# Performance work log

Hardware: AMD Instinct MI355X
Metric: run time of the kernel (lower is better)

## Reference

```python
import jax, jax.numpy as jnp
import numpy as np

N = 50000        # nodes
E = 800000       # edges (edge-nodes of the line graph)
LGE = 1600000    # line-graph edges
F_NODE = 256     # node feature dim
T = 64           # timestamp/edge feature dim
HID = 128        # hidden size
OUT = 64         # out size
SLOPE = 0.2      # leaky relu negative slope used in EdgeGCN / attention


def _glorot(key, shape):
    lim = jnp.sqrt(6.0 / (shape[0] + shape[1]))
    return jax.random.uniform(key, shape, jnp.float32, -lim, lim)


def setup_inputs() -> dict:
    key = jax.random.key(0)
    ks = jax.random.split(key, 24)
    inp = {
        "x": jax.random.normal(ks[0], (N, F_NODE), jnp.float32),
        "et": jax.random.normal(ks[1], (E, T), jnp.float32),
        "H": jax.random.randint(ks[2], (2, E), 0, N),
        "raw_edge_index": jax.random.randint(ks[3], (2, E), 0, N),
        "lg_edge_index": jax.random.randint(ks[4], (2, LGE), 0, E),
        # TSAEncoder: two SAGE-style layers on the line graph (T->HID->HID)
        "W_tsa1_s": _glorot(ks[5], (T, HID)),
        "W_tsa1_n": _glorot(ks[6], (T, HID)),
        "W_tsa2_s": _glorot(ks[7], (HID, HID)),
        "W_tsa2_n": _glorot(ks[8], (HID, HID)),
        # EdgeToNodeConv + EdgeGCN output linear
        "W_etn": _glorot(ks[9], (HID, HID)),
        "W_eg_lin": _glorot(ks[10], (HID, HID)),
        # edge_aggr SAGE (num_layers-1 = 1 layer)
        "W_ea_s": _glorot(ks[11], (HID, HID)),
        "W_ea_n": _glorot(ks[12], (HID, HID)),
        # attr_node_model SAGE (2 layers)
        "W_an1_s": _glorot(ks[13], (F_NODE, HID)),
        "W_an1_n": _glorot(ks[14], (F_NODE, HID)),
        "W_an2_s": _glorot(ks[15], (HID, HID)),
        "W_an2_n": _glorot(ks[16], (HID, HID)),
        # MixAttention
        "Wq": _glorot(ks[17], (HID, HID)),
        "Wk": _glorot(ks[18], (HID, HID)),
        "Wv": _glorot(ks[19], (HID, HID)),
        # final classifier
        "W_out": _glorot(ks[20], (HID, OUT)),
    }
    return inp


def _sage(h, src, dst, Ws, Wn, n):
    # mean-aggregator SAGE conv: self transform + mean of in-neighbors
    deg = jnp.clip(jax.ops.segment_sum(jnp.ones(src.shape[0], h.dtype), dst, num_segments=n), 1.0)
    nbr = jax.ops.segment_sum(h[src], dst, num_segments=n) / deg[:, None]
    return h @ Ws + nbr @ Wn


def reference(x, et, H, raw_edge_index, lg_edge_index,
              W_tsa1_s, W_tsa1_n, W_tsa2_s, W_tsa2_n,
              W_etn, W_eg_lin, W_ea_s, W_ea_n,
              W_an1_s, W_an1_n, W_an2_s, W_an2_n,
              Wq, Wk, Wv, W_out):
    src_lg, dst_lg = lg_edge_index[0], lg_edge_index[1]
    src, dst = raw_edge_index[0], raw_edge_index[1]

    # ---- EdgeGCN: TSAEncoder over line graph (edges as nodes) ----
    h = jax.nn.relu(_sage(et, src_lg, dst_lg, W_tsa1_s, W_tsa1_n, E))
    h = _sage(h, src_lg, dst_lg, W_tsa2_s, W_tsa2_n, E)          # [E, HID]

    # ---- EdgeToNodeConv: scatter edge reprs to both incident nodes (mean) ----
    ones_e = jnp.ones(E, h.dtype)
    agg = (jax.ops.segment_sum(h, H[0], num_segments=N)
           + jax.ops.segment_sum(h, H[1], num_segments=N))        # [N, HID]
    deg = jnp.clip(jax.ops.segment_sum(ones_e, H[0], num_segments=N)
                   + jax.ops.segment_sum(ones_e, H[1], num_segments=N), 1.0)
    node_e = (agg / deg[:, None]) @ W_etn
    edge_repr = jax.nn.leaky_relu(node_e, negative_slope=SLOPE) @ W_eg_lin  # [N, HID]

    # ---- edge_aggr: 1-layer SAGE over raw graph ----
    aggr_edge = _sage(edge_repr, src, dst, W_ea_s, W_ea_n, N)     # [N, HID]

    # ---- attr_node_model: 2-layer SAGE ----
    hn = jax.nn.relu(_sage(x, src, dst, W_an1_s, W_an1_n, N))
    hn = _sage(hn, src, dst, W_an2_s, W_an2_n, N)                 # [N, HID]

    # ---- MixAttention: edge-indexed cross attention (node queries, edge-repr keys/values) ----
    q = hn @ Wq
    k = aggr_edge @ Wk
    v = aggr_edge @ Wv
    score = jax.nn.leaky_relu(
        jnp.sum(q[dst] * k[src], axis=-1) / jnp.sqrt(jnp.asarray(HID, q.dtype)),
        negative_slope=SLOPE)                                     # [E]
    m = jax.ops.segment_max(score, dst, num_segments=N)
    m = jnp.where(jnp.isfinite(m), m, 0.0)
    ex = jnp.exp(score - m[dst])
    den = jnp.clip(jax.ops.segment_sum(ex, dst, num_segments=N), 1e-9)
    alpha = ex / den[dst]
    out = hn + jax.ops.segment_sum(alpha[:, None] * v[src], dst, num_segments=N)

    return jax.nn.log_softmax(out @ W_out, axis=1)                # [N, OUT]
```

## Files before the change

kernel.cpp:

```cpp
#include <hip/hip_runtime.h>
#include <cstddef>

static constexpr int Nn   = 50000;
static constexpr int Ee   = 800000;
static constexpr int LGEe = 1600000;

typedef __attribute__((ext_vector_type(8))) short bf16x8;
typedef __attribute__((ext_vector_type(4))) float f32x4;

__device__ __forceinline__ float bf2f(unsigned int u16) {
  return __uint_as_float(u16 << 16);
}
__device__ __forceinline__ unsigned int f2bf(float f) {
  unsigned int u = __float_as_uint(f);
  u += 0x7fffu + ((u >> 16) & 1u);
  return u >> 16;
}

__global__ __launch_bounds__(256)
void k_count_direct(const int* __restrict__ idx, int* __restrict__ cnt, int n) {
  int i = blockIdx.x * 256 + threadIdx.x;
  if (i < n) atomicAdd(&cnt[idx[i]], 1);
}
__global__ __launch_bounds__(256)
void k_count_comp(const int* __restrict__ Hrow, const int* __restrict__ dlg,
                  int* __restrict__ cnt, int n) {
  int i = blockIdx.x * 256 + threadIdx.x;
  if (i < n) atomicAdd(&cnt[Hrow[dlg[i]]], 1);
}
__global__ __launch_bounds__(256)
void k_scan1(const int* __restrict__ in, int* __restrict__ out,
             int* __restrict__ bsum, int n) {
  __shared__ int sd[256];
  int tid = threadIdx.x;
  int base = blockIdx.x * 1024 + tid * 4;
  int4 v = {0, 0, 0, 0};
  if (base < n) v = *(const int4*)(in + base);
  int s = v.x + v.y + v.z + v.w;
  sd[tid] = s; __syncthreads();
  for (int off = 1; off < 256; off <<= 1) {
    int t_ = (tid >= off) ? sd[tid - off] : 0; __syncthreads();
    sd[tid] += t_; __syncthreads();
  }
  int excl = sd[tid] - s;
  if (base < n) {
    int4 o; o.x = excl; o.y = o.x + v.x; o.z = o.y + v.y; o.w = o.z + v.z;
    *(int4*)(out + base) = o;
  }
  if (tid == 255) bsum[blockIdx.x] = sd[255];
}
__global__ __launch_bounds__(1024)
void k_scan2(int* __restrict__ b, int nb) {
  __shared__ int sd[1024];
  int tid = threadIdx.x;
  int v = (tid < nb) ? b[tid] : 0;
  sd[tid] = v; __syncthreads();
  for (int off = 1; off < 1024; off <<= 1) {
    int t_ = (tid >= off) ? sd[tid - off] : 0; __syncthreads();
    sd[tid] += t_; __syncthreads();
  }
  if (tid < nb) b[tid] = sd[tid] - v;
}
__global__ __launch_bounds__(256)
void k_scan3(int* __restrict__ out, const int* __restrict__ bsum, int n, int total) {
  int i = blockIdx.x * 256 + threadIdx.x;
  if (i < n) out[i] += bsum[i >> 10];
  if (i == 0) out[n] = total;
}
__global__ __launch_bounds__(256)
void k_fillA(const int* __restrict__ dlg, const int* __restrict__ slg,
             const int* __restrict__ ptr, int* __restrict__ cur,
             int* __restrict__ ent, int n) {
  int m = blockIdx.x * 256 + threadIdx.x;
  if (m >= n) return;
  int d = dlg[m];
  int pos = ptr[d] + atomicAdd(&cur[d], 1);
  ent[pos] = slg[m];
}
__global__ __launch_bounds__(256)
void k_fillB(const int* __restrict__ Hrow, const int* __restrict__ dlg,
             const int* __restrict__ slg, const int* __restrict__ ptrA,
             const int* __restrict__ ptrB, int* __restrict__ cur,
             int* __restrict__ entS, float* __restrict__ entW, int n) {
  int m = blockIdx.x * 256 + threadIdx.x;
  if (m >= n) return;
  int d = dlg[m];
  int seg = Hrow[d];
  int pos = ptrB[seg] + atomicAdd(&cur[seg], 1);
  entS[pos] = slg[m];
  int la = ptrA[d + 1] - ptrA[d];
  entW[pos] = 1.0f / (float)max(la, 1);
}
__global__ __launch_bounds__(256)
void k_fillC(const int* __restrict__ Hrow, const int* __restrict__ ptr,
             int* __restrict__ cur, int* __restrict__ ent, int n) {
  int e = blockIdx.x * 256 + threadIdx.x;
  if (e >= n) return;
  int seg = Hrow[e];
  int pos = ptr[seg] + atomicAdd(&cur[seg], 1);
  ent[pos] = e;
}
__global__ __launch_bounds__(256)
void k_fillD(const int* __restrict__ dstA, const int* __restrict__ srcA,
             const int* __restrict__ ptr, int* __restrict__ cur,
             int* __restrict__ ent, int n) {
  int e = blockIdx.x * 256 + threadIdx.x;
  if (e >= n) return;
  int seg = dstA[e];
  int pos = ptr[seg] + atomicAdd(&cur[seg], 1);
  ent[pos] = srcA[e];
}
__global__ __launch_bounds__(256)
void k_rdeg(const int* __restrict__ ptr, float* __restrict__ r, int n) {
  int i = blockIdx.x * 256 + threadIdx.x;
  if (i < n) r[i] = 1.0f / fmaxf((float)(ptr[i + 1] - ptr[i]), 1.0f);
}

__global__ __launch_bounds__(256)
void k_gemm128(int M, const float* __restrict__ A, int K,
               const float* __restrict__ W, const float* __restrict__ dgA,
               int reluA, int act, float* __restrict__ C)
{
  __shared__ float sA[32][132];
  __shared__ float sW[32][132];
  const int t = threadIdx.x, tr = t >> 4, tc = t & 15;
  const int row0 = blockIdx.x * 128;
  float acc[8][8];
  #pragma unroll
  for (int i = 0; i < 8; ++i)
    #pragma unroll
    for (int j = 0; j < 8; ++j) acc[i][j] = 0.f;

  #pragma unroll 1
  for (int k0 = 0; k0 < K; k0 += 32) {
    __syncthreads();
    #pragma unroll
    for (int j = 0; j < 4; ++j) {
      int idx = t * 4 + j * 1024;
      int r = idx >> 5, kk = idx & 31;
      int gr = row0 + r; if (gr > M - 1) gr = M - 1;
      float4 va = *(const float4*)(A + (size_t)gr * K + k0 + kk);
      if (reluA) {
        va.x = fmaxf(va.x, 0.f); va.y = fmaxf(va.y, 0.f);
        va.z = fmaxf(va.z, 0.f); va.w = fmaxf(va.w, 0.f);
      }
      if (dgA) {
        float sc = dgA[gr];
        va.x *= sc; va.y *= sc; va.z *= sc; va.w *= sc;
      }
      sA[kk + 0][r] = va.x; sA[kk + 1][r] = va.y;
      sA[kk + 2][r] = va.z; sA[kk + 3][r] = va.w;
    }
    #pragma unroll
    for (int j = 0; j < 4; ++j) {
      int idx = t * 4 + j * 1024;
      int kk = idx >> 7, c = idx & 127;
      *(float4*)&sW[kk][c] = *(const float4*)(W + (size_t)(k0 + kk) * 128 + c);
    }
    __syncthreads();
    #pragma unroll
    for (int kk = 0; kk < 32; ++kk) {
      float a[8], w[8];
      *(float4*)&a[0] = *(const float4*)&sA[kk][tr * 4];
      *(float4*)&a[4] = *(const float4*)&sA[kk][64 + tr * 4];
      *(float4*)&w[0] = *(const float4*)&sW[kk][tc * 4];
      *(float4*)&w[4] = *(const float4*)&sW[kk][64 + tc * 4];
      #pragma unroll
      for (int i = 0; i < 8; ++i)
        #pragma unroll
        for (int j = 0; j < 8; ++j)
          acc[i][j] = fmaf(a[i], w[j], acc[i][j]);
    }
  }
  #pragma unroll 1
  for (int i = 0; i < 8; ++i) {
    int gr = row0 + (i & 4) * 16 + tr * 4 + (i & 3);
    if (gr >= M) continue;
    float o[8];
    #pragma unroll
    for (int j = 0; j < 8; ++j) {
      float vv = acc[i][j];
      if (act == 1)      vv = fmaxf(vv, 0.f);
      else if (act == 2) vv = vv > 0.f ? vv : vv * 0.2f;
      o[j] = vv;
    }
    float* p = C + (size_t)gr * 128;
    *(float4*)(p + tc * 4)      = *(const float4*)&o[0];
    *(float4*)(p + 64 + tc * 4) = *(const float4*)&o[4];
  }
}

__global__ __launch_bounds__(256)
void k_tsa1(const float* __restrict__ et,
            const int* __restrict__ rp, const int* __restrict__ ent,
            const float* __restrict__ Ws, const float* __restrict__ Wn,
            unsigned short* __restrict__ BUF)
{
  __shared__ __align__(16) unsigned char smem[34816];
  unsigned short* sAh = (unsigned short*)smem;
  unsigned short* sAl = (unsigned short*)(smem + 16384);
  int*   sEnt  = (int*)(smem + 32768);
  float* stage = (float*)smem;

  const int t = threadIdx.x, wv = t >> 6, lane = t & 63;
  const int tr = t >> 4, tc = t & 15;
  const int nrow = lane & 15, kg = lane >> 4;
  const int seg0 = blockIdx.x * 64;
  const int segbase = seg0 + wv * 16;

  int rpv = (lane <= 16) ? rp[segbase + lane] : 0;
  int nxtv = __shfl(rpv, (lane + 1) & 63);
  float invv = 1.f / fmaxf((float)(nxtv - rpv), 1.f);

  const int base = rp[seg0];
  const int cnt  = rp[seg0 + 64] - base;
  const int lim  = cnt < 512 ? cnt : 512;
  for (int i = t; i < lim; i += 256) sEnt[i] = ent[base + i];

  {
    float dv[16];
    #pragma unroll
    for (int i = 0; i < 16; ++i)
      dv[i] = et[(size_t)(segbase + i) * 64 + lane];
    #pragma unroll
    for (int i = 0; i < 16; ++i) {
      int ss = wv * 16 + i;
      unsigned int hi = f2bf(dv[i]);
      float lo = dv[i] - bf2f(hi);
      int idx = ss * 128 + (lane ^ ((ss & 7) << 3));
      sAh[idx] = (unsigned short)hi;
      sAl[idx] = (unsigned short)f2bf(lo);
    }
  }

  bf16x8 Bh[2][4], Bl[2][4];
  #pragma unroll
  for (int np = 0; np < 2; ++np) {
    int n = (wv * 2 + np) * 16 + nrow;
    #pragma unroll
    for (int kc = 0; kc < 4; ++kc) {
      const float* Wp = (kc < 2) ? Ws : Wn;
      int kr0 = (kc & 1) * 32 + kg * 8;
      #pragma unroll
      for (int j = 0; j < 8; ++j) {
        float w = Wp[(size_t)(kr0 + j) * 128 + n];
        unsigned int hi = f2bf(w);
        float lo = w - bf2f(hi);
        Bh[np][kc][j] = (short)(unsigned short)hi;
        Bl[np][kc][j] = (short)(unsigned short)f2bf(lo);
      }
    }
  }
  __syncthreads();

  {
    int q0 = __shfl(rpv, 0);
    int q1 = __shfl(rpv, 16);
    int c = 0;
    int b_next = __shfl(rpv, 1);
    float idg = __shfl(invv, 0);
    float a = 0.f;
    #pragma unroll 1
    for (int j = q0; j < q1; j += 8) {
      float x[8];
      #pragma unroll
      for (int u = 0; u < 8; ++u) {
        int jj = j + u; jj = jj < q1 ? jj : q1 - 1;
        int ix = jj - base;
        int s = (ix < 512) ? sEnt[ix] : ent[jj];
        x[u] = et[(size_t)s * 64 + lane];
      }
      #pragma unroll
      for (int u = 0; u < 8; ++u) {
        int jj = j + u;
        if (jj >= q1) break;
        while (jj >= b_next) {
          float v = a * idg;
          int ss = wv * 16 + c;
          unsigned int hi = f2bf(v);
          float lo = v - bf2f(hi);
          int idx = ss * 128 + ((64 + lane) ^ ((ss & 7) << 3));
          sAh[idx] = (unsigned short)hi;
          sAl[idx] = (unsigned short)f2bf(lo);
          a = 0.f;
          ++c;
          b_next = __shfl(rpv, c + 1);
          idg = __shfl(invv, c);
        }
        a += x[u];
      }
    }
    #pragma unroll 1
    for (;;) {
      float v = a * idg;
      int ss = wv * 16 + c;
      unsigned int hi = f2bf(v);
      float lo = v - bf2f(hi);
      int idx = ss * 128 + ((64 + lane) ^ ((ss & 7) << 3));
      sAh[idx] = (unsigned short)hi;
      sAl[idx] = (unsigned short)f2bf(lo);
      a = 0.f;
      if (++c >= 16) break;
      idg = __shfl(invv, c);
    }
  }
  __syncthreads();

  f32x4 acc[4][2];
  #pragma unroll
  for (int m = 0; m < 4; ++m)
    #pragma unroll
    for (int np = 0; np < 2; ++np)
      acc[m][np] = (f32x4){0.f, 0.f, 0.f, 0.f};

  #pragma unroll
  for (int kc = 0; kc < 4; ++kc) {
    #pragma unroll
    for (int m = 0; m < 4; ++m) {
      int ss = m * 16 + nrow;
      int kbase = kc * 32 + kg * 8;
      int idx = ss * 128 + (kbase ^ ((ss & 7) << 3));
      bf16x8 ah = *(const bf16x8*)(sAh + idx);
      bf16x8 al = *(const bf16x8*)(sAl + idx);
      #pragma unroll
      for (int np = 0; np < 2; ++np) {
        acc[m][np] = __builtin_amdgcn_mfma_f32_16x16x32_bf16(ah, Bh[np][kc], acc[m][np], 0, 0, 0);
        acc[m][np] = __builtin_amdgcn_mfma_f32_16x16x32_bf16(al, Bh[np][kc], acc[m][np], 0, 0, 0);
        acc[m][np] = __builtin_amdgcn_mfma_f32_16x16x32_bf16(ah, Bl[np][kc], acc[m][np], 0, 0, 0);
      }
    }
  }

  __syncthreads();
  #pragma unroll
  for (int m = 0; m < 4; ++m)
    #pragma unroll
    for (int np = 0; np < 2; ++np)
      #pragma unroll
      for (int r = 0; r < 4; ++r)
        stage[(m * 16 + kg * 4 + r) * 132 + (wv * 2 + np) * 16 + nrow] = acc[m][np][r];
  __syncthreads();
  #pragma unroll
  for (int i = 0; i < 4; ++i) {
    int s = tr * 4 + i;
    const float* sp = stage + s * 132 + tc * 8;
    float4 v0 = *(const float4*)sp;
    float4 v1 = *(const float4*)(sp + 4);
    unsigned int pk[4];
    pk[0] = f2bf(v0.x) | (f2bf(v0.y) << 16);
    pk[1] = f2bf(v0.z) | (f2bf(v0.w) << 16);
    pk[2] = f2bf(v1.x) | (f2bf(v1.y) << 16);
    pk[3] = f2bf(v1.z) | (f2bf(v1.w) << 16);
    uint4 st = {pk[0], pk[1], pk[2], pk[3]};
    *(uint4*)(BUF + (size_t)(seg0 + s) * 128 + tc * 8) = st;
  }
}

__global__ __launch_bounds__(256)
void k_gg2(int nseg, const int* __restrict__ rp, const int* __restrict__ ent,
           const float* __restrict__ entw, int segscale,
           const unsigned short* __restrict__ SRC, const float* __restrict__ W,
           float* __restrict__ OUT, int beta)
{
  __shared__ float sA[128][34];
  __shared__ float sW[32][132];
  __shared__ int sEnt[1024];
  const int t = threadIdx.x, wv = t >> 6, lane = t & 63;
  const int tr = t >> 4, tc = t & 15;
  const int seg0 = blockIdx.x * 32;
  const int segbase = seg0 + wv * 8;
  int idxl = segbase + lane;
  int rpv = (lane <= 8 && idxl <= nseg) ? rp[idxl] : 0;
  int nxt = __shfl(rpv, (lane + 1) & 63);
  float invv = 1.f / fmaxf((float)(nxt - rpv), 1.f);

  const int base = rp[seg0];
  int endseg = seg0 + 32; if (endseg > nseg) endseg = nseg;
  const int cnt = rp[endseg] - base;
  const int lim = cnt < 1024 ? cnt : 1024;
  for (int i = t; i < lim; i += 256) sEnt[i] = ent[base + i];
  __syncthreads();

  {
    int q0 = __shfl(rpv, 0), q1 = __shfl(rpv, 8);
    int c = 0;
    int b_next = __shfl(rpv, 1);
    float a0 = 0.f, a1 = 0.f;
    #pragma unroll 1
    for (int j = q0; j < q1; j += 8) {
      int ids[8];
      unsigned int u[8];
      float w[8];
      #pragma unroll
      for (int uu = 0; uu < 8; ++uu) {
        int jj = j + uu; jj = jj < q1 ? jj : q1 - 1;
        int ix = jj - base;
        ids[uu] = (ix < 1024) ? sEnt[ix] : ent[jj];
      }
      #pragma unroll
      for (int uu = 0; uu < 8; ++uu)
        u[uu] = *(const unsigned int*)(SRC + (size_t)ids[uu] * 128 + 2 * lane);
      if (entw) {
        #pragma unroll
        for (int uu = 0; uu < 8; ++uu) {
          int jj = j + uu; jj = jj < q1 ? jj : q1 - 1;
          w[uu] = entw[jj];
        }
      }
      #pragma unroll
      for (int uu = 0; uu < 8; ++uu) {
        int jj = j + uu;
        if (jj >= q1) break;
        while (jj >= b_next) {
          float s0 = a0, s1 = a1;
          if (segscale) { float sc = __shfl(invv, c); s0 *= sc; s1 *= sc; }
          int col = wv * 8 + c;
          sA[2 * lane][col]     = s0;
          sA[2 * lane + 1][col] = s1;
          a0 = a1 = 0.f;
          ++c;
          b_next = __shfl(rpv, c + 1);
        }
        float wj = entw ? w[uu] : 1.f;
        a0 = fmaf(wj, fmaxf(bf2f(u[uu] & 0xffffu), 0.f), a0);
        a1 = fmaf(wj, fmaxf(bf2f(u[uu] >> 16),     0.f), a1);
      }
    }
    #pragma unroll 1
    for (;;) {
      float s0 = a0, s1 = a1;
      if (segscale) { float sc = __shfl(invv, c); s0 *= sc; s1 *= sc; }
      int col = wv * 8 + c;
      sA[2 * lane][col]     = s0;
      sA[2 * lane + 1][col] = s1;
      a0 = a1 = 0.f;
      if (++c >= 8) break;
    }
  }
  __syncthreads();

  float acc[2][8];
  #pragma unroll
  for (int i = 0; i < 2; ++i)
    #pragma unroll
    for (int j = 0; j < 8; ++j) acc[i][j] = 0.f;

  #pragma unroll 1
  for (int k0 = 0; k0 < 128; k0 += 32) {
    #pragma unroll
    for (int j = 0; j < 4; ++j) {
      int idx = t * 4 + j * 1024;
      int kk = idx >> 7, c = idx & 127;
      *(float4*)&sW[kk][c] = *(const float4*)(W + (size_t)(k0 + kk) * 128 + c);
    }
    __syncthreads();
    #pragma unroll
    for (int kk = 0; kk < 32; ++kk) {
      float a2[2], w8[8];
      *(float2*)&a2[0] = *(const float2*)&sA[k0 + kk][tr * 2];
      *(float4*)&w8[0] = *(const float4*)&sW[kk][tc * 4];
      *(float4*)&w8[4] = *(const float4*)&sW[kk][64 + tc * 4];
      #pragma unroll
      for (int i = 0; i < 2; ++i)
        #pragma unroll
        for (int j = 0; j < 8; ++j)
          acc[i][j] = fmaf(a2[i], w8[j], acc[i][j]);
    }
    __syncthreads();
  }

  #pragma unroll
  for (int i = 0; i < 2; ++i) {
    int seg = seg0 + tr * 2 + i;
    if (seg >= nseg) continue;
    float o[8];
    #pragma unroll
    for (int j = 0; j < 8; ++j) o[j] = acc[i][j];
    float* p = OUT + (size_t)seg * 128;
    if (beta) {
      float4 c0 = *(const float4*)(p + tc * 4), c1 = *(const float4*)(p + 64 + tc * 4);
      o[0] += c0.x; o[1] += c0.y; o[2] += c0.z; o[3] += c0.w;
      o[4] += c1.x; o[5] += c1.y; o[6] += c1.z; o[7] += c1.w;
    }
    *(float4*)(p + tc * 4)      = *(const float4*)&o[0];
    *(float4*)(p + 64 + tc * 4) = *(const float4*)&o[4];
  }
}

__global__ __launch_bounds__(256)
void k_gsum(const int* __restrict__ rp, const int* __restrict__ ent,
            const float* __restrict__ SRC, float* __restrict__ O, int nseg)
{
  int wv = threadIdx.x >> 6, lane = threadIdx.x & 63;
  int seg = blockIdx.x * 4 + wv;
  if (seg >= nseg) return;
  int p0 = rp[seg], p1 = rp[seg + 1];
  if (p0 >= p1) return;
  float a0 = 0.f, a1 = 0.f;
  #pragma unroll 1
  for (int j = p0; j < p1; j += 8) {
    int ids[8];
    #pragma unroll
    for (int i = 0; i < 8; ++i) {
      int jj = j + i; jj = jj < p1 ? jj : p1 - 1;
      ids[i] = ent[jj];
    }
    float2 v[8];
    #pragma unroll
    for (int i = 0; i < 8; ++i)
      v[i] = ((const float2*)(SRC + (size_t)ids[i] * 128))[lane];
    #pragma unroll
    for (int i = 0; i < 8; ++i) {
      bool ok = (j + i) < p1;
      a0 += ok ? v[i].x : 0.f;
      a1 += ok ? v[i].y : 0.f;
    }
  }
  float sc = 1.f / fmaxf((float)(p1 - p0), 1.f);
  float2* orow = (float2*)(O + (size_t)seg * 128);
  float2 cur = orow[lane];
  cur.x += a0 * sc; cur.y += a1 * sc;
  orow[lane] = cur;
}

__global__ __launch_bounds__(256)
void k_attn(const int* __restrict__ rp, const int* __restrict__ ent,
            const float* __restrict__ q, const float* __restrict__ kb,
            const float* __restrict__ vb, float* __restrict__ o, int nseg)
{
  int wv = threadIdx.x >> 6, lane = threadIdx.x & 63;
  int seg = blockIdx.x * 4 + wv;
  if (seg >= nseg) return;
  int p0 = rp[seg], p1 = rp[seg + 1];
  if (p0 >= p1) return;
  float2 q2 = ((const float2*)(q + (size_t)seg * 128))[lane];
  float m = -1e30f, l = 0.f, o0 = 0.f, o1 = 0.f;
  #pragma unroll 1
  for (int j = p0; j < p1; j += 4) {
    int s[4];
    #pragma unroll
    for (int i = 0; i < 4; ++i) {
      int jj = j + i; jj = jj < p1 ? jj : p1 - 1;
      s[i] = ent[jj];
    }
    float2 k2[4], v2[4];
    #pragma unroll
    for (int i = 0; i < 4; ++i)
      k2[i] = ((const float2*)(kb + (size_t)s[i] * 128))[lane];
    #pragma unroll
    for (int i = 0; i < 4; ++i)
      v2[i] = ((const float2*)(vb + (size_t)s[i] * 128))[lane];
    float d[4];
    #pragma unroll
    for (int i = 0; i < 4; ++i) d[i] = fmaf(q2.x, k2[i].x, q2.y * k2[i].y);
    #pragma unroll
    for (int off = 1; off < 64; off <<= 1) {
      #pragma unroll
      for (int i = 0; i < 4; ++i) d[i] += __shfl_xor(d[i], off);
    }
    float sc[4];
    #pragma unroll
    for (int i = 0; i < 4; ++i) {
      float v = d[i] * 0.088388347648318447f;
      v = v > 0.f ? v : 0.2f * v;
      sc[i] = (j + i < p1) ? v : -1e30f;
    }
    float mb = fmaxf(fmaxf(sc[0], sc[1]), fmaxf(sc[2], sc[3]));
    float mn = fmaxf(m, mb);
    float scale = expf(m - mn);
    float e[4];
    #pragma unroll
    for (int i = 0; i < 4; ++i)
      e[i] = (j + i < p1) ? expf(sc[i] - mn) : 0.f;
    l  = l  * scale + ((e[0] + e[1]) + (e[2] + e[3]));
    o0 = o0 * scale + ((e[0] * v2[0].x + e[1] * v2[1].x) + (e[2] * v2[2].x + e[3] * v2[3].x));
    o1 = o1 * scale + ((e[0] * v2[0].y + e[1] * v2[1].y) + (e[2] * v2[2].y + e[3] * v2[3].y));
    m = mn;
  }
  float inv = 1.f / fmaxf(l, 1e-9f);
  float2* orow = (float2*)(o + (size_t)seg * 128);
  float2 cur = orow[lane];
  cur.x += o0 * inv; cur.y += o1 * inv;
  orow[lane] = cur;
}

__global__ __launch_bounds__(256)
void k_out(const float* __restrict__ attn, const float* __restrict__ Wout,
           float* __restrict__ out, int n) {
  __shared__ float sW[128 * 64];
  for (int i = threadIdx.x; i < 128 * 64; i += 256) sW[i] = Wout[i];
  __syncthreads();
  int wave = threadIdx.x >> 6, lane = threadIdx.x & 63;
  int row = blockIdx.x * 4 + wave;
  if (row >= n) return;
  const float* a = attn + (size_t)row * 128;
  float z = 0.f;
  #pragma unroll 8
  for (int k = 0; k < 128; ++k) z = fmaf(a[k], sW[k * 64 + lane], z);
  float mx = z;
  #pragma unroll
  for (int off = 32; off; off >>= 1) mx = fmaxf(mx, __shfl_xor(mx, off));
  float ee = expf(z - mx);
  float ss = ee;
  #pragma unroll
  for (int off = 32; off; off >>= 1) ss += __shfl_xor(ss, off);
  out[(size_t)row * 64 + lane] = z - mx - logf(ss);
}

extern "C" void kernel_launch(void* const* d_in, const int* in_sizes, int n_in,
                              void* d_out, int out_size, void* d_ws, size_t ws_size,
                              hipStream_t stream) {
  (void)in_sizes; (void)n_in; (void)out_size;
  const float* x        = (const float*)d_in[0];
  const float* et       = (const float*)d_in[1];
  const int*   H0       = (const int*)d_in[2];
  const int*   H1       = H0 + Ee;
  const int*   src      = (const int*)d_in[3];
  const int*   dst      = src + Ee;
  const int*   src_lg   = (const int*)d_in[4];
  const int*   dst_lg   = src_lg + LGEe;
  const float* W_tsa1_s = (const float*)d_in[5];
  const float* W_tsa1_n = (const float*)d_in[6];
  const float* W_tsa2_s = (const float*)d_in[7];
  const float* W_tsa2_n = (const float*)d_in[8];
  const float* W_etn    = (const float*)d_in[9];
  const float* W_eg_lin = (const float*)d_in[10];
  const float* W_ea_s   = (const float*)d_in[11];
  const float* W_ea_n   = (const float*)d_in[12];
  const float* W_an1_s  = (const float*)d_in[13];
  const float* W_an1_n  = (const float*)d_in[14];
  const float* W_an2_s  = (const float*)d_in[15];
  const float* W_an2_n  = (const float*)d_in[16];
  const float* Wq       = (const float*)d_in[17];
  const float* Wk       = (const float*)d_in[18];
  const float* Wv       = (const float*)d_in[19];
  const float* W_out    = (const float*)d_in[20];
  float* out = (float*)d_out;

  char* wp = (char*)d_ws;
  size_t avail = ws_size;
  auto alloc = [&](size_t bytes) -> void* {
    void* r = (void*)wp;
    size_t pad = (bytes + 255) & ~(size_t)255;
    wp += pad; avail = (avail >= pad) ? avail - pad : 0;
    return r;
  };
  const size_t NH = (size_t)Nn * 128;
  unsigned short* BUF = (unsigned short*)alloc((size_t)Ee * 128 * 2);
  float* agg   = (float*)alloc(NH * 4);
  int* ptrA  = (int*)alloc(((size_t)Ee + 1) * 4);
  int* cntA  = (int*)alloc((size_t)Ee * 4);
  int* entA  = (int*)alloc((size_t)LGEe * 4);
  int* ptrB  = (int*)alloc(((size_t)Nn + 1) * 4);
  int* cntB  = (int*)alloc((size_t)Nn * 4);
  int* entBs = (int*)alloc((size_t)2 * LGEe * 4);
  float* entBw = (float*)alloc((size_t)2 * LGEe * 4);
  int* ptrC  = (int*)alloc(((size_t)Nn + 1) * 4);
  int* cntC  = (int*)alloc((size_t)Nn * 4);
  int* entC  = (int*)alloc((size_t)2 * Ee * 4);
  int* ptrD  = (int*)alloc(((size_t)Nn + 1) * 4);
  int* cntD  = (int*)alloc((size_t)Nn * 4);
  int* entD  = (int*)alloc((size_t)Ee * 4);
  float* rdegN = (float*)alloc((size_t)Nn * 4);
  int* bsum  = (int*)alloc(2048 * 4);
  if (avail == 0 && wp > (char*)d_ws + ws_size) return;

  float* er  = (float*)BUF + 0 * NH;
  float* ae  = (float*)BUF + 1 * NH;
  float* hn  = (float*)BUF + 2 * NH;
  float* hn2 = (float*)BUF + 3 * NH;
  float* qb  = (float*)BUF + 4 * NH;
  float* kb  = (float*)BUF + 5 * NH;
  float* vb  = (float*)BUF + 6 * NH;
  float* tmp = (float*)BUF + 7 * NH;

  auto cdiv = [](long a, long b) { return (int)((a + b - 1) / b); };
  auto scan = [&](int* cnt, int* ptr, int n, int total) {
    int nb = cdiv(n, 1024);
    k_scan1<<<nb, 256, 0, stream>>>(cnt, ptr, bsum, n);
    k_scan2<<<1, 1024, 0, stream>>>(bsum, nb);
    k_scan3<<<cdiv(n, 256), 256, 0, stream>>>(ptr, bsum, n, total);
  };

  const int gLG = cdiv(LGEe, 256), gEe = cdiv(Ee, 256);

  hipMemsetAsync(cntA, 0, (size_t)Ee * 4, stream);
  k_count_direct<<<gLG, 256, 0, stream>>>(dst_lg, cntA, LGEe);
  scan(cntA, ptrA, Ee, LGEe);
  hipMemsetAsync(cntA, 0, (size_t)Ee * 4, stream);
  k_fillA<<<gLG, 256, 0, stream>>>(dst_lg, src_lg, ptrA, cntA, entA, LGEe);

  hipMemsetAsync(cntB, 0, (size_t)Nn * 4, stream);
  k_count_comp<<<gLG, 256, 0, stream>>>(H0, dst_lg, cntB, LGEe);
  k_count_comp<<<gLG, 256, 0, stream>>>(H1, dst_lg, cntB, LGEe);
  scan(cntB, ptrB, Nn, 2 * LGEe);
  hipMemsetAsync(cntB, 0, (size_t)Nn * 4, stream);
  k_fillB<<<gLG, 256, 0, stream>>>(H0, dst_lg, src_lg, ptrA, ptrB, cntB, entBs, entBw, LGEe);
  k_fillB<<<gLG, 256, 0, stream>>>(H1, dst_lg, src_lg, ptrA, ptrB, cntB, entBs, entBw, LGEe);

  hipMemsetAsync(cntC, 0, (size_t)Nn * 4, stream);
  k_count_direct<<<gEe, 256, 0, stream>>>(H0, cntC, Ee);
  k_count_direct<<<gEe, 256, 0, stream>>>(H1, cntC, Ee);
  scan(cntC, ptrC, Nn, 2 * Ee);
  hipMemsetAsync(cntC, 0, (size_t)Nn * 4, stream);
  k_fillC<<<gEe, 256, 0, stream>>>(H0, ptrC, cntC, entC, Ee);
  k_fillC<<<gEe, 256, 0, stream>>>(H1, ptrC, cntC, entC, Ee);

  hipMemsetAsync(cntD, 0, (size_t)Nn * 4, stream);
  k_count_direct<<<gEe, 256, 0, stream>>>(dst, cntD, Ee);
  scan(cntD, ptrD, Nn, Ee);
  hipMemsetAsync(cntD, 0, (size_t)Nn * 4, stream);
  k_fillD<<<gEe, 256, 0, stream>>>(dst, src, ptrD, cntD, entD, Ee);
  k_rdeg<<<cdiv(Nn, 256), 256, 0, stream>>>(ptrC, rdegN, Nn);

  const int gN128 = cdiv(Nn, 128);
  const int gN32  = cdiv(Nn, 32);
  const int gW    = cdiv(Nn, 4);

  k_tsa1<<<Ee / 64, 256, 0, stream>>>(et, ptrA, entA, W_tsa1_s, W_tsa1_n, BUF);

  k_gg2<<<gN32, 256, 0, stream>>>(Nn, ptrC, entC, nullptr, 0, BUF, W_tsa2_s, agg, 0);
  k_gg2<<<gN32, 256, 0, stream>>>(Nn, ptrB, entBs, entBw, 0, BUF, W_tsa2_n, agg, 1);
  k_gemm128<<<gN128, 256, 0, stream>>>(Nn, agg, 128, W_etn, rdegN, 0, 2, tmp);
  k_gemm128<<<gN128, 256, 0, stream>>>(Nn, tmp, 128, W_eg_lin, nullptr, 0, 0, er);

  k_gemm128<<<gN128, 256, 0, stream>>>(Nn, er, 128, W_ea_s, nullptr, 0, 0, ae);
  k_gemm128<<<gN128, 256, 0, stream>>>(Nn, er, 128, W_ea_n, nullptr, 0, 0, tmp);
  k_gsum<<<gW, 256, 0, stream>>>(ptrD, entD, tmp, ae, Nn);

  k_gemm128<<<gN128, 256, 0, stream>>>(Nn, x, 256, W_an1_s, nullptr, 0, 0, hn);
  k_gemm128<<<gN128, 256, 0, stream>>>(Nn, x, 256, W_an1_n, nullptr, 0, 0, tmp);
  k_gsum<<<gW, 256, 0, stream>>>(ptrD, entD, tmp, hn, Nn);
  k_gemm128<<<gN128, 256, 0, stream>>>(Nn, hn, 128, W_an2_s, nullptr, 1, 0, hn2);
  k_gemm128<<<gN128, 256, 0, stream>>>(Nn, hn, 128, W_an2_n, nullptr, 1, 0, tmp);
  k_gsum<<<gW, 256, 0, stream>>>(ptrD, entD, tmp, hn2, Nn);

  k_gemm128<<<gN128, 256, 0, stream>>>(Nn, hn2, 128, Wq, nullptr, 0, 0, qb);
  k_gemm128<<<gN128, 256, 0, stream>>>(Nn, ae, 128, Wk, nullptr, 0, 0, kb);
  k_gemm128<<<gN128, 256, 0, stream>>>(Nn, ae, 128, Wv, nullptr, 0, 0, vb);
  k_attn<<<gW, 256, 0, stream>>>(ptrD, entD, qb, kb, vb, hn2, Nn);

  k_out<<<gW, 256, 0, stream>>>(hn2, W_out, out, Nn);
}
```

Before: 2.855 ms.

## Replace segment-per-wave gathers with edge-balanced chunked pooling and separate GEMMs

```diff
diff --git a/kernel.cpp b/kernel.cpp
--- a/kernel.cpp
+++ b/kernel.cpp
@@ -119,7 +119,7 @@
 __global__ __launch_bounds__(256)
 void k_gemm128(int M, const float* __restrict__ A, int K,
                const float* __restrict__ W, const float* __restrict__ dgA,
-               int reluA, int act, float* __restrict__ C)
+               int reluA, int act, float* __restrict__ C, int beta)
 {
   __shared__ float sA[32][132];
   __shared__ float sW[32][132];
@@ -185,6 +185,11 @@
       o[j] = vv;
     }
     float* p = C + (size_t)gr * 128;
+    if (beta) {
+      float4 c0 = *(const float4*)(p + tc * 4), c1 = *(const float4*)(p + 64 + tc * 4);
+      o[0] += c0.x; o[1] += c0.y; o[2] += c0.z; o[3] += c0.w;
+      o[4] += c1.x; o[5] += c1.y; o[6] += c1.z; o[7] += c1.w;
+    }
     *(float4*)(p + tc * 4)      = *(const float4*)&o[0];
     *(float4*)(p + 64 + tc * 4) = *(const float4*)&o[4];
   }
@@ -357,170 +362,136 @@
 }
 
 __global__ __launch_bounds__(256)
-void k_gg2(int nseg, const int* __restrict__ rp, const int* __restrict__ ent,
-           const float* __restrict__ entw, int segscale,
-           const unsigned short* __restrict__ SRC, const float* __restrict__ W,
-           float* __restrict__ OUT, int beta)
+void k_poolb(const int* __restrict__ rp, const int* __restrict__ ent,
+             const float* __restrict__ entw,
+             const unsigned short* __restrict__ SRC,
+             float* __restrict__ O, int nseg, int total)
 {
-  __shared__ float sA[128][34];
-  __shared__ float sW[32][132];
-  __shared__ int sEnt[1024];
-  const int t = threadIdx.x, wv = t >> 6, lane = t & 63;
-  const int tr = t >> 4, tc = t & 15;
-  const int seg0 = blockIdx.x * 32;
-  const int segbase = seg0 + wv * 8;
-  int idxl = segbase + lane;
-  int rpv = (lane <= 8 && idxl <= nseg) ? rp[idxl] : 0;
-  int nxt = __shfl(rpv, (lane + 1) & 63);
-  float invv = 1.f / fmaxf((float)(nxt - rpv), 1.f);
-
-  const int base = rp[seg0];
-  int endseg = seg0 + 32; if (endseg > nseg) endseg = nseg;
-  const int cnt = rp[endseg] - base;
-  const int lim = cnt < 1024 ? cnt : 1024;
-  for (int i = t; i < lim; i += 256) sEnt[i] = ent[base + i];
-  __syncthreads();
-
+  const int wv = threadIdx.x >> 6, lane = threadIdx.x & 63;
+  const int chunk = blockIdx.x * 4 + wv;
+  const int c0 = chunk * 256;
+  if (c0 >= total) return;
+  int c1 = c0 + 256; if (c1 > total) c1 = total;
+
+  int lo = 0, hi = nseg;
+  while (lo + 1 < hi) {
+    int mid = (lo + hi) >> 1;
+    if (rp[mid] <= c0) lo = mid; else hi = mid;
+  }
+  int seg = lo;
+  int sstart = rp[seg];
+  int send = rp[seg + 1];
+  float a0 = 0.f, a1 = 0.f;
+
+  #pragma unroll 1
+  for (int j = c0; j < c1; j += 8) {
+    int ids[8]; float w[8];
+    #pragma unroll
+    for (int u = 0; u < 8; ++u) {
+      int jj = j + u; jj = jj < c1 ? jj : c1 - 1;
+      ids[u] = ent[jj];
+      w[u] = entw ? entw[jj] : 1.f;
+    }
+    unsigned int uv[8];
+    #pragma unroll
+    for (int u = 0; u < 8; ++u)
+      uv[u] = *(const unsigned int*)(SRC + (size_t)ids[u] * 128 + 2 * lane);
+    #pragma unroll
+    for (int u = 0; u < 8; ++u) {
+      int jj = j + u;
+      if (jj >= c1) break;
+      while (jj >= send) {
+        float* p = O + (size_t)seg * 128;
+        if (sstart >= c0 && send <= c1) {
+          p[2 * lane]     += a0;
+          p[2 * lane + 1] += a1;
+        } else {
+          atomicAdd(p + 2 * lane, a0);
+          atomicAdd(p + 2 * lane + 1, a1);
+        }
+        a0 = a1 = 0.f;
+        ++seg; sstart = send; send = rp[seg + 1];
+      }
+      a0 = fmaf(w[u], fmaxf(bf2f(uv[u] & 0xffffu), 0.f), a0);
+      a1 = fmaf(w[u], fmaxf(bf2f(uv[u] >> 16),     0.f), a1);
+    }
+  }
   {
-    int q0 = __shfl(rpv, 0), q1 = __shfl(rpv, 8);
-    int c = 0;
-    int b_next = __shfl(rpv, 1);
-    float a0 = 0.f, a1 = 0.f;
-    #pragma unroll 1
-    for (int j = q0; j < q1; j += 8) {
-      int ids[8];
-      unsigned int u[8];
-      float w[8];
-      #pragma unroll
-      for (int uu = 0; uu < 8; ++uu) {
-        int jj = j + uu; jj = jj < q1 ? jj : q1 - 1;
-        int ix = jj - base;
-        ids[uu] = (ix < 1024) ? sEnt[ix] : ent[jj];
+    float* p = O + (size_t)seg * 128;
+    if (sstart >= c0 && send <= c1) {
+      p[2 * lane]     += a0;
+      p[2 * lane + 1] += a1;
+    } else {
+      atomicAdd(p + 2 * lane, a0);
+      atomicAdd(p + 2 * lane + 1, a1);
+    }
+  }
+}
+
+__global__ __launch_bounds__(256)
+void k_poolf(const int* __restrict__ rp, const int* __restrict__ ent,
+             const float* __restrict__ SRC, float* __restrict__ O,
+             int nseg, int total)
+{
+  const int wv = threadIdx.x >> 6, lane = threadIdx.x & 63;
+  const int chunk = blockIdx.x * 4 + wv;
+  const int c0 = chunk * 256;
+  if (c0 >= total) return;
+  int c1 = c0 + 256; if (c1 > total) c1 = total;
+
+  int lo = 0, hi = nseg;
+  while (lo + 1 < hi) {
+    int mid = (lo + hi) >> 1;
+    if (rp[mid] <= c0) lo = mid; else hi = mid;
+  }
+  int seg = lo;
+  int sstart = rp[seg];
+  int send = rp[seg + 1];
+  float a0 = 0.f, a1 = 0.f;
+
+  #pragma unroll 1
+  for (int j = c0; j < c1; j += 8) {
+    int ids[8];
+    #pragma unroll
+    for (int u = 0; u < 8; ++u) {
+      int jj = j + u; jj = jj < c1 ? jj : c1 - 1;
+      ids[u] = ent[jj];
+    }
+    float2 v[8];
+    #pragma unroll
+    for (int u = 0; u < 8; ++u)
+      v[u] = ((const float2*)(SRC + (size_t)ids[u] * 128))[lane];
+    #pragma unroll
+    for (int u = 0; u < 8; ++u) {
+      int jj = j + u;
+      if (jj >= c1) break;
+      while (jj >= send) {
+        float sc = 1.f / fmaxf((float)(send - sstart), 1.f);
+        float* p = O + (size_t)seg * 128;
+        if (sstart >= c0 && send <= c1) {
+          p[2 * lane]     += a0 * sc;
+          p[2 * lane + 1] += a1 * sc;
+        } else {
+          atomicAdd(p + 2 * lane, a0 * sc);
+          atomicAdd(p + 2 * lane + 1, a1 * sc);
+        }
+        a0 = a1 = 0.f;
+        ++seg; sstart = send; send = rp[seg + 1];
       }
-      #pragma unroll
-      for (int uu = 0; uu < 8; ++uu)
-        u[uu] = *(const unsigned int*)(SRC + (size_t)ids[uu] * 128 + 2 * lane);
-      if (entw) {
-        #pragma unroll
-        for (int uu = 0; uu < 8; ++uu) {
-          int jj = j + uu; jj = jj < q1 ? jj : q1 - 1;
-          w[uu] = entw[jj];
-        }
-      }
-      #pragma unroll
-      for (int uu = 0; uu < 8; ++uu) {
-        int jj = j + uu;
-        if (jj >= q1) break;
-        while (jj >= b_next) {
-          float s0 = a0, s1 = a1;
-          if (segscale) { float sc = __shfl(invv, c); s0 *= sc; s1 *= sc; }
-          int col = wv * 8 + c;
-          sA[2 * lane][col]     = s0;
-          sA[2 * lane + 1][col] = s1;
-          a0 = a1 = 0.f;
-          ++c;
-          b_next = __shfl(rpv, c + 1);
-        }
-        float wj = entw ? w[uu] : 1.f;
-        a0 = fmaf(wj, fmaxf(bf2f(u[uu] & 0xffffu), 0.f), a0);
-        a1 = fmaf(wj, fmaxf(bf2f(u[uu] >> 16),     0.f), a1);
-      }
-    }
-    #pragma unroll 1
-    for (;;) {
-      float s0 = a0, s1 = a1;
-      if (segscale) { float sc = __shfl(invv, c); s0 *= sc; s1 *= sc; }
-      int col = wv * 8 + c;
-      sA[2 * lane][col]     = s0;
-      sA[2 * lane + 1][col] = s1;
-      a0 = a1 = 0.f;
-      if (++c >= 8) break;
-    }
-  }
-  __syncthreads();
-
-  float acc[2][8];
-  #pragma unroll
-  for (int i = 0; i < 2; ++i)
-    #pragma unroll
-    for (int j = 0; j < 8; ++j) acc[i][j] = 0.f;
-
-  #pragma unroll 1
-  for (int k0 = 0; k0 < 128; k0 += 32) {
-    #pragma unroll
-    for (int j = 0; j < 4; ++j) {
-      int idx = t * 4 + j * 1024;
-      int kk = idx >> 7, c = idx & 127;
-      *(float4*)&sW[kk][c] = *(const float4*)(W + (size_t)(k0 + kk) * 128 + c);
-    }
-    __syncthreads();
-    #pragma unroll
-    for (int kk = 0; kk < 32; ++kk) {
-      float a2[2], w8[8];
-      *(float2*)&a2[0] = *(const float2*)&sA[k0 + kk][tr * 2];
-      *(float4*)&w8[0] = *(const float4*)&sW[kk][tc * 4];
-      *(float4*)&w8[4] = *(const float4*)&sW[kk][64 + tc * 4];
-      #pragma unroll
-      for (int i = 0; i < 2; ++i)
-        #pragma unroll
-        for (int j = 0; j < 8; ++j)
-          acc[i][j] = fmaf(a2[i], w8[j], acc[i][j]);
-    }
-    __syncthreads();
-  }
-
-  #pragma unroll
-  for (int i = 0; i < 2; ++i) {
-    int seg = seg0 + tr * 2 + i;
-    if (seg >= nseg) continue;
-    float o[8];
-    #pragma unroll
-    for (int j = 0; j < 8; ++j) o[j] = acc[i][j];
-    float* p = OUT + (size_t)seg * 128;
-    if (beta) {
-      float4 c0 = *(const float4*)(p + tc * 4), c1 = *(const float4*)(p + 64 + tc * 4);
-      o[0] += c0.x; o[1] += c0.y; o[2] += c0.z; o[3] += c0.w;
-      o[4] += c1.x; o[5] += c1.y; o[6] += c1.z; o[7] += c1.w;
-    }
-    *(float4*)(p + tc * 4)      = *(const float4*)&o[0];
-    *(float4*)(p + 64 + tc * 4) = *(const float4*)&o[4];
-  }
-}
-
-__global__ __launch_bounds__(256)
-void k_gsum(const int* __restrict__ rp, const int* __restrict__ ent,
-            const float* __restrict__ SRC, float* __restrict__ O, int nseg)
-{
-  int wv = threadIdx.x >> 6, lane = threadIdx.x & 63;
-  int seg = blockIdx.x * 4 + wv;
-  if (seg >= nseg) return;
-  int p0 = rp[seg], p1 = rp[seg + 1];
-  if (p0 >= p1) return;
-  float a0 = 0.f, a1 = 0.f;
-  #pragma unroll 1
-  for (int j = p0; j < p1; j += 8) {
-    int ids[8];
-    #pragma unroll
-    for (int i = 0; i < 8; ++i) {
-      int jj = j + i; jj = jj < p1 ? jj : p1 - 1;
-      ids[i] = ent[jj];
-    }
-    float2 v[8];
-    #pragma unroll
-    for (int i = 0; i < 8; ++i)
-      v[i] = ((const float2*)(SRC + (size_t)ids[i] * 128))[lane];
-    #pragma unroll
-    for (int i = 0; i < 8; ++i) {
-      bool ok = (j + i) < p1;
-      a0 += ok ? v[i].x : 0.f;
-      a1 += ok ? v[i].y : 0.f;
-    }
-  }
-  float sc = 1.f / fmaxf((float)(p1 - p0), 1.f);
-  float2* orow = (float2*)(O + (size_t)seg * 128);
-  float2 cur = orow[lane];
-  cur.x += a0 * sc; cur.y += a1 * sc;
-  orow[lane] = cur;
+      a0 += v[u].x; a1 += v[u].y;
+    }
+  }
+  {
+    float sc = 1.f / fmaxf((float)(send - sstart), 1.f);
+    float* p = O + (size_t)seg * 128;
+    if (sstart >= c0 && send <= c1) {
+      p[2 * lane]     += a0 * sc;
+      p[2 * lane + 1] += a1 * sc;
+    } else {
+      atomicAdd(p + 2 * lane, a0 * sc);
+      atomicAdd(p + 2 * lane + 1, a1 * sc);
+    }
+  }
 }
 
 __global__ __launch_bounds__(256)
@@ -673,6 +644,7 @@
   float* kb  = (float*)BUF + 5 * NH;
   float* vb  = (float*)BUF + 6 * NH;
   float* tmp = (float*)BUF + 7 * NH;
+  float* T = (float*)entBs;
 
   auto cdiv = [](long a, long b) { return (int)((a + b - 1) / b); };
   auto scan = [&](int* cnt, int* ptr, int n, int total) {
@@ -714,30 +686,36 @@
   k_rdeg<<<cdiv(Nn, 256), 256, 0, stream>>>(ptrC, rdegN, Nn);
 
   const int gN128 = cdiv(Nn, 128);
-  const int gN32  = cdiv(Nn, 32);
   const int gW    = cdiv(Nn, 4);
+  const int gP2   = cdiv(cdiv(2 * LGEe, 256), 4);
+  const int gP1   = cdiv(cdiv(2 * Ee, 256), 4);
+  const int gPf   = cdiv(cdiv(Ee, 256), 4);
 
   k_tsa1<<<Ee / 64, 256, 0, stream>>>(et, ptrA, entA, W_tsa1_s, W_tsa1_n, BUF);
 
-  k_gg2<<<gN32, 256, 0, stream>>>(Nn, ptrC, entC, nullptr, 0, BUF, W_tsa2_s, agg, 0);
-  k_gg2<<<gN32, 256, 0, stream>>>(Nn, ptrB, entBs, entBw, 0, BUF, W_tsa2_n, agg, 1);
-  k_gemm128<<<gN128, 256, 0, stream>>>(Nn, agg, 128, W_etn, rdegN, 0, 2, tmp);
-  k_gemm128<<<gN128, 256, 0, stream>>>(Nn, tmp, 128, W_eg_lin, nullptr, 0, 0, er);
-
-  k_gemm128<<<gN128, 256, 0, stream>>>(Nn, er, 128, W_ea_s, nullptr, 0, 0, ae);
-  k_gemm128<<<gN128, 256, 0, stream>>>(Nn, er, 128, W_ea_n, nullptr, 0, 0, tmp);
-  k_gsum<<<gW, 256, 0, stream>>>(ptrD, entD, tmp, ae, Nn);
-
-  k_gemm128<<<gN128, 256, 0, stream>>>(Nn, x, 256, W_an1_s, nullptr, 0, 0, hn);
-  k_gemm128<<<gN128, 256, 0, stream>>>(Nn, x, 256, W_an1_n, nullptr, 0, 0, tmp);
-  k_gsum<<<gW, 256, 0, stream>>>(ptrD, entD, tmp, hn, Nn);
-  k_gemm128<<<gN128, 256, 0, stream>>>(Nn, hn, 128, W_an2_s, nullptr, 1, 0, hn2);
-  k_gemm128<<<gN128, 256, 0, stream>>>(Nn, hn, 128, W_an2_n, nullptr, 1, 0, tmp);
-  k_gsum<<<gW, 256, 0, stream>>>(ptrD, entD, tmp, hn2, Nn);
-
-  k_gemm128<<<gN128, 256, 0, stream>>>(Nn, hn2, 128, Wq, nullptr, 0, 0, qb);
-  k_gemm128<<<gN128, 256, 0, stream>>>(Nn, ae, 128, Wk, nullptr, 0, 0, kb);
-  k_gemm128<<<gN128, 256, 0, stream>>>(Nn, ae, 128, Wv, nullptr, 0, 0, vb);
+  hipMemsetAsync(agg, 0, NH * 4, stream);
+  k_poolb<<<gP2, 256, 0, stream>>>(ptrB, entBs, entBw, BUF, agg, Nn, 2 * LGEe);
+  k_gemm128<<<gN128, 256, 0, stream>>>(Nn, agg, 128, W_tsa2_n, nullptr, 0, 0, T, 0);
+  hipMemsetAsync(agg, 0, NH * 4, stream);
+  k_poolb<<<gP1, 256, 0, stream>>>(ptrC, entC, nullptr, BUF, agg, Nn, 2 * Ee);
+  k_gemm128<<<gN128, 256, 0, stream>>>(Nn, agg, 128, W_tsa2_s, nullptr, 0, 0, T, 1);
+  k_gemm128<<<gN128, 256, 0, stream>>>(Nn, T, 128, W_etn, rdegN, 0, 2, tmp, 0);
+  k_gemm128<<<gN128, 256, 0, stream>>>(Nn, tmp, 128, W_eg_lin, nullptr, 0, 0, er, 0);
+
+  k_gemm128<<<gN128, 256, 0, stream>>>(Nn, er, 128, W_ea_s, nullptr, 0, 0, ae, 0);
+  k_gemm128<<<gN128, 256, 0, stream>>>(Nn, er, 128, W_ea_n, nullptr, 0, 0, tmp, 0);
+  k_poolf<<<gPf, 256, 0, stream>>>(ptrD, entD, tmp, ae, Nn, Ee);
+
+  k_gemm128<<<gN128, 256, 0, stream>>>(Nn, x, 256, W_an1_s, nullptr, 0, 0, hn, 0);
+  k_gemm128<<<gN128, 256, 0, stream>>>(Nn, x, 256, W_an1_n, nullptr, 0, 0, tmp, 0);
+  k_poolf<<<gPf, 256, 0, stream>>>(ptrD, entD, tmp, hn, Nn, Ee);
+  k_gemm128<<<gN128, 256, 0, stream>>>(Nn, hn, 128, W_an2_s, nullptr, 1, 0, hn2, 0);
+  k_gemm128<<<gN128, 256, 0, stream>>>(Nn, hn, 128, W_an2_n, nullptr, 1, 0, tmp, 0);
+  k_poolf<<<gPf, 256, 0, stream>>>(ptrD, entD, tmp, hn2, Nn, Ee);
+
+  k_gemm128<<<gN128, 256, 0, stream>>>(Nn, hn2, 128, Wq, nullptr, 0, 0, qb, 0);
+  k_gemm128<<<gN128, 256, 0, stream>>>(Nn, ae, 128, Wk, nullptr, 0, 0, kb, 0);
+  k_gemm128<<<gN128, 256, 0, stream>>>(Nn, ae, 128, Wv, nullptr, 0, 0, vb, 0);
   k_attn<<<gW, 256, 0, stream>>>(ptrD, entD, qb, kb, vb, hn2, Nn);
 
   k_out<<<gW, 256, 0, stream>>>(hn2, W_out, out, Nn);
```

Result: no change. 2.812 ms (-1.5%).
